# Optimization experiments

Measured on AMD Instinct MI355X. Metric: run time of the kernel, lower is better.

Reference implementation:

```python
import jax, jax.numpy as jnp
import numpy as np

V = 8001
H = 512
B = 64
T = 129  # seq len; model unrolls T-1 steps
EPS = 1e-5
P_DROP = 0.3


def setup_inputs() -> dict:
    key = jax.random.key(0)
    ks = jax.random.split(key, 16)
    s = 1.0 / np.sqrt(H)
    inp = {
        "x": jax.random.randint(ks[0], (B, T), 0, V),
        "emb": jax.random.normal(ks[1], (V, H), jnp.float32) * 0.1,
        "W_ih1": jax.random.normal(ks[2], (4 * H, H), jnp.float32) * s,
        "W_hh1": jax.random.normal(ks[3], (4 * H, H), jnp.float32) * s,
        "b_ih1": jax.random.normal(ks[4], (4 * H,), jnp.float32) * s,
        "b_hh1": jax.random.normal(ks[5], (4 * H,), jnp.float32) * s,
        "gamma1": jnp.ones((H,), jnp.float32),
        "beta1": jnp.zeros((H,), jnp.float32),
        "mask1": (jax.random.bernoulli(ks[6], 1 - P_DROP, (B, H)).astype(jnp.float32) / (1 - P_DROP)),
        "W_ih2": jax.random.normal(ks[7], (4 * H, H), jnp.float32) * s,
        "W_hh2": jax.random.normal(ks[8], (4 * H, H), jnp.float32) * s,
        "b_ih2": jax.random.normal(ks[9], (4 * H,), jnp.float32) * s,
        "b_hh2": jax.random.normal(ks[10], (4 * H,), jnp.float32) * s,
        "gamma2": jnp.ones((H,), jnp.float32),
        "beta2": jnp.zeros((H,), jnp.float32),
        "mask2": (jax.random.bernoulli(ks[11], 1 - P_DROP, (B, H)).astype(jnp.float32) / (1 - P_DROP)),
        "W_dec": jax.random.normal(ks[12], (V, H), jnp.float32) * s,
        "b_dec": jax.random.normal(ks[13], (V,), jnp.float32) * s,
    }
    return inp


def _lstm_cell(xt, h, c, W_ih, W_hh, b_ih, b_hh):
    # PyTorch LSTMCell gate packing: i, f, g, o
    gates = xt @ W_ih.T + b_ih + h @ W_hh.T + b_hh  # [B, 4H]
    i, f, g, o = jnp.split(gates, 4, axis=-1)
    c_new = jax.nn.sigmoid(f) * c + jax.nn.sigmoid(i) * jnp.tanh(g)
    h_new = jax.nn.sigmoid(o) * jnp.tanh(c_new)
    return h_new, c_new


def _batchnorm(h, gamma, beta):
    # training-mode BatchNorm1d: biased batch stats over batch dim
    mu = h.mean(axis=0)
    var = h.var(axis=0)
    return gamma * (h - mu) * jax.lax.rsqrt(var + EPS) + beta


def reference(x, emb, W_ih1, W_hh1, b_ih1, b_hh1, gamma1, beta1, mask1,
              W_ih2, W_hh2, b_ih2, b_hh2, gamma2, beta2, mask2, W_dec, b_dec):
    embed = emb[x]                              # [B, T, H]
    xs = jnp.swapaxes(embed[:, :-1, :], 0, 1)   # [T-1, B, H]

    def step(carry, xt):
        h1, c1, h2, c2 = carry
        h1, c1 = _lstm_cell(xt, h1, c1, W_ih1, W_hh1, b_ih1, b_hh1)
        a = _batchnorm(h1, gamma1, beta1) * mask1
        h2, c2 = _lstm_cell(a, h2, c2, W_ih2, W_hh2, b_ih2, b_hh2)
        b = _batchnorm(h2, gamma2, beta2) * mask2
        out = b @ W_dec.T + b_dec               # [B, V]
        return (h1, c1, h2, c2), out

    z = jnp.zeros((B, H), embed.dtype)
    _, outs = jax.lax.scan(step, (z, z, z, z), xs)  # [T-1, B, V]
    return jnp.transpose(outs, (1, 2, 0))           # [B, V, T-1]
```

## Files before the change

### kernel.cpp

```cpp
#include <hip/hip_runtime.h>

typedef __attribute__((ext_vector_type(8))) short bf16x8;
typedef __attribute__((ext_vector_type(4))) float f32x4;

#define NBATCH 64
#define NH     512
#define NV     8001
#define NVP    8064
#define NSTEP  128
#define NG     2048
#define SLAB   32768

#define OFF_XS    ((size_t)0)
#define SZ_XS     ((size_t)NSTEP*SLAB*2)
#define OFF_WP    (OFF_XS + SZ_XS)
#define SZ_WP     ((size_t)2*2048*1024*2)
#define OFF_WDEC  (OFF_WP + SZ_WP)
#define SZ_WDEC   ((size_t)NVP*NH*2)
#define OFF_BIAS  (OFF_WDEC + SZ_WDEC)
#define SZ_BIAS   ((size_t)2*NG*4)
#define OFF_H1    (OFF_BIAS + SZ_BIAS)
#define SZ_H1     ((size_t)(NSTEP+1)*SLAB*2)
#define OFF_AB    (OFF_H1 + SZ_H1)
#define SZ_AB     ((size_t)NSTEP*SLAB*2)
#define OFF_H2    (OFF_AB + SZ_AB)
#define SZ_H2     ((size_t)(NSTEP+1)*SLAB*2)
#define OFF_BSEQ  (OFF_H2 + SZ_H2)
#define SZ_BSEQ   ((size_t)NSTEP*SLAB*2)
#define OFF_BAR   (OFF_BSEQ + SZ_BSEQ)
#define SZ_BAR    ((size_t)32768)

__device__ __forceinline__ unsigned short f2bf(float x) {
  union { float f; unsigned u; } v; v.f = x;
  unsigned r = v.u + 0x7FFFu + ((v.u >> 16) & 1u);
  return (unsigned short)(r >> 16);
}
__device__ __forceinline__ float sigm(float x) { return 1.f / (1.f + __expf(-x)); }

template <int SLP>
__device__ __forceinline__ void waitflag(unsigned* f) {
  while (__hip_atomic_load(f, __ATOMIC_RELAXED, __HIP_MEMORY_SCOPE_AGENT) < 32u)
    __builtin_amdgcn_s_sleep(SLP);
  asm volatile("" ::: "memory");
}


__global__ void k_xs(const int* __restrict__ x, const float* __restrict__ emb,
                     unsigned short* __restrict__ xs) {
  int idx = blockIdx.x * 256 + threadIdx.x;
  int t = idx >> 12, b = (idx >> 6) & 63, h8 = idx & 63;
  const float* src = emb + (size_t)x[b * 129 + t] * NH + h8 * 8;
  float4 a = *(const float4*)src, c = *(const float4*)(src + 4);
  unsigned short tmp[8] = {f2bf(a.x), f2bf(a.y), f2bf(a.z), f2bf(a.w),
                           f2bf(c.x), f2bf(c.y), f2bf(c.z), f2bf(c.w)};
  *(uint4*)(xs + (size_t)idx * 8) = *(const uint4*)tmp;
}

__global__ void k_wdec(const float* __restrict__ W, unsigned short* __restrict__ wdec) {
  int idx = blockIdx.x * 256 + threadIdx.x;
  int v = idx >> 6, h8 = idx & 63;
  unsigned short tmp[8] = {0, 0, 0, 0, 0, 0, 0, 0};
  if (v < NV) {
    const float* src = W + (size_t)v * NH + h8 * 8;
    float4 a = *(const float4*)src, c = *(const float4*)(src + 4);
    tmp[0] = f2bf(a.x); tmp[1] = f2bf(a.y); tmp[2] = f2bf(a.z); tmp[3] = f2bf(a.w);
    tmp[4] = f2bf(c.x); tmp[5] = f2bf(c.y); tmp[6] = f2bf(c.z); tmp[7] = f2bf(c.w);
  }
  *(uint4*)(wdec + (size_t)idx * 8) = *(const uint4*)tmp;
}

__global__ void k_bias(const float* __restrict__ bi1, const float* __restrict__ bh1,
                       const float* __restrict__ bi2, const float* __restrict__ bh2,
                       float* __restrict__ bias) {
  int i = blockIdx.x * 256 + threadIdx.x;
  bias[i] = (i < NG) ? (bi1[i] + bh1[i]) : (bi2[i - NG] + bh2[i - NG]);
}

__global__ void k_wpack(const float* __restrict__ Wih1, const float* __restrict__ Whh1,
                        const float* __restrict__ Wih2, const float* __restrict__ Whh2,
                        unsigned short* __restrict__ wp) {
  int tid = blockIdx.x * 256 + threadIdx.x;
  int l = tid & 63, g = (tid >> 6) & 3, s = (tid >> 8) & 31, lb = (tid >> 13) & 31, layer = tid >> 18;
  int n = l & 15, q = l >> 4;
  int r = g * NH + lb * 16 + n;
  int k0 = s * 32 + q * 8;
  const float* Wih = layer ? Wih2 : Wih1;
  const float* Whh = layer ? Whh2 : Whh1;
  const float* src = (k0 < NH) ? (Wih + (size_t)r * NH + k0) : (Whh + (size_t)r * NH + (k0 - NH));
  unsigned short tmp[8];
#pragma unroll
  for (int j = 0; j < 8; ++j) tmp[j] = f2bf(src[j]);
  *(uint4*)(wp + (size_t)tid * 8) = *(const uint4*)tmp;
}

__global__ void __launch_bounds__(256, 1)
k_main(const unsigned short* __restrict__ xs, const unsigned short* __restrict__ wpack,
       const float* __restrict__ bias,
       const float* __restrict__ gamma1, const float* __restrict__ beta1, const float* __restrict__ mask1,
       const float* __restrict__ gamma2, const float* __restrict__ beta2, const float* __restrict__ mask2,
       unsigned short* __restrict__ h1q, unsigned short* __restrict__ abq,
       unsigned short* __restrict__ h2q, unsigned short* __restrict__ bseq,
       unsigned* __restrict__ bar,
       const unsigned short* __restrict__ wdec, const float* __restrict__ bdec,
       float* __restrict__ out) {
  __shared__ unsigned short wlds[32 * 4 * 64 * 8];
  __shared__ float red[4][2][16];

  unsigned* done1 = bar;
  unsigned* done2 = bar + 2048;
  unsigned* qcnt  = bar + 4096;

  const int bid = blockIdx.x;
  const int lane = threadIdx.x & 63, w = threadIdx.x >> 6;
  const int q = lane >> 4, n = lane & 15;

  if (bid < 64) {
    const int layer = bid >> 5, lb = bid & 31, f0 = lb * 16;
    const float* gam = layer ? gamma2 : gamma1;
    const float* bet = layer ? beta2 : beta1;
    const float* msk = layer ? mask2 : mask1;
    const float* bias_l = bias + layer * NG;

    {
      const uint4* src = (const uint4*)(wpack + (size_t)bid * (32 * 4 * 64 * 8));
      uint4* dst = (uint4*)wlds;
      for (int i = threadIdx.x; i < 32 * 4 * 64; i += 256) dst[i] = src[i];
    }
    __syncthreads();

    const int m0 = w * 16;
    const float gmv = gam[f0 + n], btv = bet[f0 + n];
    float bias_g[4], mk[4];
#pragma unroll
    for (int g = 0; g < 4; ++g) bias_g[g] = bias_l[g * NH + f0 + n];
#pragma unroll
    for (int r = 0; r < 4; ++r) mk[r] = msk[(m0 + q * 4 + r) * NH + f0 + n];

    float cst[4] = {0.f, 0.f, 0.f, 0.f};

    for (int t = 0; t < NSTEP; ++t) {
      f32x4 acc[4];
#pragma unroll
      for (int g = 0; g < 4; ++g) acc[g] = (f32x4){bias_g[g], bias_g[g], bias_g[g], bias_g[g]};

      if (layer == 0) {
        const unsigned short* rowA0 = xs + (size_t)t * SLAB + (m0 + n) * NH;
#pragma unroll
        for (int s = 0; s < 16; ++s) {
          bf16x8 af = *(const bf16x8*)(rowA0 + s * 32 + q * 8);
#pragma unroll
          for (int g = 0; g < 4; ++g)
            acc[g] = __builtin_amdgcn_mfma_f32_16x16x32_bf16(
                af, *(const bf16x8*)&wlds[((s * 4 + g) * 64 + lane) * 8], acc[g], 0, 0, 0);
        }
        if (t > 0) waitflag<1>(done1 + (t - 1) * 16);
        const unsigned short* rowA1 = h1q + (size_t)t * SLAB + (m0 + n) * NH;
#pragma unroll
        for (int s = 0; s < 16; ++s) {
          bf16x8 af = *(const bf16x8*)(rowA1 + s * 32 + q * 8);
#pragma unroll
          for (int g = 0; g < 4; ++g)
            acc[g] = __builtin_amdgcn_mfma_f32_16x16x32_bf16(
                af, *(const bf16x8*)&wlds[(((s + 16) * 4 + g) * 64 + lane) * 8], acc[g], 0, 0, 0);
        }
      } else {
        if (t > 0) waitflag<1>(done2 + (t - 1) * 16);
        const unsigned short* rowA1 = h2q + (size_t)t * SLAB + (m0 + n) * NH;
#pragma unroll
        for (int s = 0; s < 16; ++s) {
          bf16x8 af = *(const bf16x8*)(rowA1 + s * 32 + q * 8);
#pragma unroll
          for (int g = 0; g < 4; ++g)
            acc[g] = __builtin_amdgcn_mfma_f32_16x16x32_bf16(
                af, *(const bf16x8*)&wlds[(((s + 16) * 4 + g) * 64 + lane) * 8], acc[g], 0, 0, 0);
        }
        waitflag<1>(done1 + t * 16);
        const unsigned short* rowA0 = abq + (size_t)t * SLAB + (m0 + n) * NH;
#pragma unroll
        for (int s = 0; s < 16; ++s) {
          bf16x8 af = *(const bf16x8*)(rowA0 + s * 32 + q * 8);
#pragma unroll
          for (int g = 0; g < 4; ++g)
            acc[g] = __builtin_amdgcn_mfma_f32_16x16x32_bf16(
                af, *(const bf16x8*)&wlds[((s * 4 + g) * 64 + lane) * 8], acc[g], 0, 0, 0);
        }
      }

      float hv[4], sum = 0.f, ssq = 0.f;
#pragma unroll
      for (int r = 0; r < 4; ++r) {
        float ig = sigm(acc[0][r]), fg = sigm(acc[1][r]);
        float gg = tanhf(acc[2][r]), og = sigm(acc[3][r]);
        cst[r] = fg * cst[r] + ig * gg;
        hv[r] = og * tanhf(cst[r]);
        sum += hv[r]; ssq += hv[r] * hv[r];
      }
      sum += __shfl_xor(sum, 16); ssq += __shfl_xor(ssq, 16);
      sum += __shfl_xor(sum, 32); ssq += __shfl_xor(ssq, 32);
      if (q == 0) { red[w][0][n] = sum; red[w][1][n] = ssq; }
      __syncthreads();
      float s1 = red[0][0][n] + red[1][0][n] + red[2][0][n] + red[3][0][n];
      float s2 = red[0][1][n] + red[1][1][n] + red[2][1][n] + red[3][1][n];
      float mu = s1 * (1.f / 64.f);
      float var = s2 * (1.f / 64.f) - mu * mu;
      float rs = rsqrtf(var + 1e-5f);

      unsigned short* hout = ((layer == 0) ? h1q : h2q) + (size_t)(t + 1) * SLAB;
      unsigned short* aout = ((layer == 0) ? abq : bseq) + (size_t)t * SLAB;
#pragma unroll
      for (int r = 0; r < 4; ++r) {
        int row = m0 + q * 4 + r;
        float bn = (hv[r] - mu) * rs * gmv + btv;
        unsigned short hb = f2bf(hv[r]);
        unsigned short av = f2bf(bn * mk[r]);
        __hip_atomic_store(&hout[row * NH + f0 + n], hb, __ATOMIC_RELAXED, __HIP_MEMORY_SCOPE_AGENT);
        __hip_atomic_store(&aout[row * NH + f0 + n], av, __ATOMIC_RELAXED, __HIP_MEMORY_SCOPE_AGENT);
      }

      __syncthreads();
      if (threadIdx.x == 0)
        atomicAdd((layer ? done2 : done1) + t * 16, 1u);
    }
  }

  while (true) {
    unsigned c = 0;
    if (lane == 0) c = atomicAdd(qcnt, 1u);
    c = __shfl(c, 0);
    if (c >= 16384u) break;
    unsigned tc = c >> 12, r = c & 4095u;
    if (r >= 4032u) continue;
    int nb = (int)(r >> 6), b = (int)(r & 63u);
    waitflag<8>(done2 + (tc * 32 + 31) * 16);

    const int n0 = nb * 128;
    f32x4 acc[2][8];
#pragma unroll
    for (int nt = 0; nt < 8; ++nt) {
      int v = n0 + nt * 16 + n;
      float bd = (v < NV) ? bdec[v] : 0.f;
      acc[0][nt] = (f32x4){bd, bd, bd, bd};
      acc[1][nt] = acc[0][nt];
    }
    const unsigned short* arow[2];
#pragma unroll
    for (int mt = 0; mt < 2; ++mt)
      arow[mt] = bseq + ((size_t)(tc * 32 + mt * 16 + n) * NBATCH + b) * NH;
    const unsigned short* brow[8];
#pragma unroll
    for (int nt = 0; nt < 8; ++nt) brow[nt] = wdec + (size_t)(n0 + nt * 16 + n) * NH;

#pragma unroll 4
    for (int s = 0; s < 16; ++s) {
      bf16x8 af[2];
#pragma unroll
      for (int mt = 0; mt < 2; ++mt) af[mt] = *(const bf16x8*)(arow[mt] + s * 32 + q * 8);
#pragma unroll
      for (int nt = 0; nt < 8; ++nt) {
        bf16x8 bf = *(const bf16x8*)(brow[nt] + s * 32 + q * 8);
#pragma unroll
        for (int mt = 0; mt < 2; ++mt)
          acc[mt][nt] = __builtin_amdgcn_mfma_f32_16x16x32_bf16(af[mt], bf, acc[mt][nt], 0, 0, 0);
      }
    }
#pragma unroll
    for (int mt = 0; mt < 2; ++mt)
#pragma unroll
      for (int nt = 0; nt < 8; ++nt) {
        int v = n0 + nt * 16 + n;
        if (v < NV) {
          int t0 = (int)tc * 32 + mt * 16 + q * 4;
          *(f32x4*)(out + ((size_t)b * NV + v) * NSTEP + t0) = acc[mt][nt];
        }
      }
  }
}

extern "C" void kernel_launch(void* const* d_in, const int* in_sizes, int n_in,
                              void* d_out, int out_size, void* d_ws, size_t ws_size,
                              hipStream_t stream) {
  const int*   x     = (const int*)d_in[0];
  const float* emb   = (const float*)d_in[1];
  const float* Wih1  = (const float*)d_in[2];
  const float* Whh1  = (const float*)d_in[3];
  const float* bi1   = (const float*)d_in[4];
  const float* bh1   = (const float*)d_in[5];
  const float* g1    = (const float*)d_in[6];
  const float* be1   = (const float*)d_in[7];
  const float* m1    = (const float*)d_in[8];
  const float* Wih2  = (const float*)d_in[9];
  const float* Whh2  = (const float*)d_in[10];
  const float* bi2   = (const float*)d_in[11];
  const float* bh2   = (const float*)d_in[12];
  const float* g2    = (const float*)d_in[13];
  const float* be2   = (const float*)d_in[14];
  const float* m2    = (const float*)d_in[15];
  const float* Wdec  = (const float*)d_in[16];
  const float* bdec  = (const float*)d_in[17];
  float* out = (float*)d_out;
  char* ws = (char*)d_ws;

  unsigned short* xs    = (unsigned short*)(ws + OFF_XS);
  unsigned short* wp    = (unsigned short*)(ws + OFF_WP);
  unsigned short* wdec  = (unsigned short*)(ws + OFF_WDEC);
  float*          bias  = (float*)(ws + OFF_BIAS);
  unsigned short* h1q   = (unsigned short*)(ws + OFF_H1);
  unsigned short* abq   = (unsigned short*)(ws + OFF_AB);
  unsigned short* h2q   = (unsigned short*)(ws + OFF_H2);
  unsigned short* bseq  = (unsigned short*)(ws + OFF_BSEQ);
  unsigned*       bar   = (unsigned*)(ws + OFF_BAR);

  (void)hipMemsetAsync(h1q, 0, SLAB * 2, stream);
  (void)hipMemsetAsync(h2q, 0, SLAB * 2, stream);
  (void)hipMemsetAsync(bar, 0, SZ_BAR, stream);

  k_xs   <<<dim3(2048), dim3(256), 0, stream>>>(x, emb, xs);
  k_wdec <<<dim3(2016), dim3(256), 0, stream>>>(Wdec, wdec);
  k_bias <<<dim3(16),   dim3(256), 0, stream>>>(bi1, bh1, bi2, bh2, bias);
  k_wpack<<<dim3(2048), dim3(256), 0, stream>>>(Wih1, Whh1, Wih2, Whh2, wp);

  void* kargs[] = {(void*)&xs, (void*)&wp, (void*)&bias,
                   (void*)&g1, (void*)&be1, (void*)&m1,
                   (void*)&g2, (void*)&be2, (void*)&m2,
                   (void*)&h1q, (void*)&abq, (void*)&h2q, (void*)&bseq, (void*)&bar,
                   (void*)&wdec, (void*)&bdec, (void*)&out};
  (void)hipLaunchCooperativeKernel((void*)k_main, dim3(256), dim3(256), kargs, 0, stream);
}
```

Baseline: 1.684 ms.

## Fold prep kernels into cooperative main kernel and refine flag signalling

```diff
diff --git a/kernel.cpp b/kernel.cpp
--- a/kernel.cpp
+++ b/kernel.cpp
@@ -28,7 +28,13 @@
 #define OFF_BSEQ  (OFF_H2 + SZ_H2)
 #define SZ_BSEQ   ((size_t)NSTEP*SLAB*2)
 #define OFF_BAR   (OFF_BSEQ + SZ_BSEQ)
-#define SZ_BAR    ((size_t)32768)
+#define SZ_BAR    ((size_t)65536)
+
+#define F_D1(t)   ((t) * 32)
+#define F_D2(t)   (4096 + (t) * 32)
+#define F_QCNT    8192
+#define F_GBAR    8224
+#define F_DRDY(c) (8320 + (c) * 32)
 
 __device__ __forceinline__ unsigned short f2bf(float x) {
   union { float f; unsigned u; } v; v.f = x;
@@ -44,85 +50,98 @@
   asm volatile("" ::: "memory");
 }
 
-
-__global__ void k_xs(const int* __restrict__ x, const float* __restrict__ emb,
-                     unsigned short* __restrict__ xs) {
-  int idx = blockIdx.x * 256 + threadIdx.x;
-  int t = idx >> 12, b = (idx >> 6) & 63, h8 = idx & 63;
-  const float* src = emb + (size_t)x[b * 129 + t] * NH + h8 * 8;
-  float4 a = *(const float4*)src, c = *(const float4*)(src + 4);
-  unsigned short tmp[8] = {f2bf(a.x), f2bf(a.y), f2bf(a.z), f2bf(a.w),
-                           f2bf(c.x), f2bf(c.y), f2bf(c.z), f2bf(c.w)};
-  *(uint4*)(xs + (size_t)idx * 8) = *(const uint4*)tmp;
-}
-
-__global__ void k_wdec(const float* __restrict__ W, unsigned short* __restrict__ wdec) {
-  int idx = blockIdx.x * 256 + threadIdx.x;
-  int v = idx >> 6, h8 = idx & 63;
-  unsigned short tmp[8] = {0, 0, 0, 0, 0, 0, 0, 0};
-  if (v < NV) {
-    const float* src = W + (size_t)v * NH + h8 * 8;
-    float4 a = *(const float4*)src, c = *(const float4*)(src + 4);
-    tmp[0] = f2bf(a.x); tmp[1] = f2bf(a.y); tmp[2] = f2bf(a.z); tmp[3] = f2bf(a.w);
-    tmp[4] = f2bf(c.x); tmp[5] = f2bf(c.y); tmp[6] = f2bf(c.z); tmp[7] = f2bf(c.w);
-  }
-  *(uint4*)(wdec + (size_t)idx * 8) = *(const uint4*)tmp;
-}
-
-__global__ void k_bias(const float* __restrict__ bi1, const float* __restrict__ bh1,
-                       const float* __restrict__ bi2, const float* __restrict__ bh2,
-                       float* __restrict__ bias) {
-  int i = blockIdx.x * 256 + threadIdx.x;
-  bias[i] = (i < NG) ? (bi1[i] + bh1[i]) : (bi2[i - NG] + bh2[i - NG]);
-}
-
-__global__ void k_wpack(const float* __restrict__ Wih1, const float* __restrict__ Whh1,
-                        const float* __restrict__ Wih2, const float* __restrict__ Whh2,
-                        unsigned short* __restrict__ wp) {
-  int tid = blockIdx.x * 256 + threadIdx.x;
-  int l = tid & 63, g = (tid >> 6) & 3, s = (tid >> 8) & 31, lb = (tid >> 13) & 31, layer = tid >> 18;
-  int n = l & 15, q = l >> 4;
-  int r = g * NH + lb * 16 + n;
-  int k0 = s * 32 + q * 8;
-  const float* Wih = layer ? Wih2 : Wih1;
-  const float* Whh = layer ? Whh2 : Whh1;
-  const float* src = (k0 < NH) ? (Wih + (size_t)r * NH + k0) : (Whh + (size_t)r * NH + (k0 - NH));
-  unsigned short tmp[8];
-#pragma unroll
-  for (int j = 0; j < 8; ++j) tmp[j] = f2bf(src[j]);
-  *(uint4*)(wp + (size_t)tid * 8) = *(const uint4*)tmp;
-}
-
-__global__ void __launch_bounds__(256, 1)
-k_main(const unsigned short* __restrict__ xs, const unsigned short* __restrict__ wpack,
-       const float* __restrict__ bias,
-       const float* __restrict__ gamma1, const float* __restrict__ beta1, const float* __restrict__ mask1,
-       const float* __restrict__ gamma2, const float* __restrict__ beta2, const float* __restrict__ mask2,
-       unsigned short* __restrict__ h1q, unsigned short* __restrict__ abq,
-       unsigned short* __restrict__ h2q, unsigned short* __restrict__ bseq,
-       unsigned* __restrict__ bar,
-       const unsigned short* __restrict__ wdec, const float* __restrict__ bdec,
-       float* __restrict__ out) {
+template <int SLP>
+__device__ __forceinline__ void waitone(unsigned* f) {
+  if (!__hip_atomic_load(f, __ATOMIC_RELAXED, __HIP_MEMORY_SCOPE_AGENT)) {
+    do { __builtin_amdgcn_s_sleep(SLP); }
+    while (!__hip_atomic_load(f, __ATOMIC_RELAXED, __HIP_MEMORY_SCOPE_AGENT));
+  }
+  asm volatile("" ::: "memory");
+}
+
+struct KArgs {
+  const int* x; const float* emb;
+  const float* Wih1; const float* Whh1; const float* bi1; const float* bh1;
+  const float* g1; const float* be1; const float* m1;
+  const float* Wih2; const float* Whh2; const float* bi2; const float* bh2;
+  const float* g2; const float* be2; const float* m2;
+  const float* Wdec; const float* bdec;
+  unsigned short* xs; unsigned short* wp; unsigned short* wdec; float* bias;
+  unsigned short* h1q; unsigned short* abq; unsigned short* h2q; unsigned short* bseq;
+  unsigned* bar; float* out;
+};
+
+__global__ void __launch_bounds__(256, 1) k_main(KArgs a) {
   __shared__ unsigned short wlds[32 * 4 * 64 * 8];
   __shared__ float red[4][2][16];
 
-  unsigned* done1 = bar;
-  unsigned* done2 = bar + 2048;
-  unsigned* qcnt  = bar + 4096;
-
+  unsigned* bar = a.bar;
   const int bid = blockIdx.x;
   const int lane = threadIdx.x & 63, w = threadIdx.x >> 6;
   const int q = lane >> 4, n = lane & 15;
 
+  {
+    const int gtid = bid * 256 + threadIdx.x;
+    if (gtid < 4096)
+      a.bias[gtid] = (gtid < NG) ? (a.bi1[gtid] + a.bh1[gtid])
+                                 : (a.bi2[gtid - NG] + a.bh2[gtid - NG]);
+    if (gtid < 4096) {
+      ((uint4*)a.h1q)[gtid] = (uint4){0, 0, 0, 0};
+      ((uint4*)a.h2q)[gtid] = (uint4){0, 0, 0, 0};
+    }
+    for (int i = gtid; i < 524288; i += 65536) {
+      int t = i >> 12, b = (i >> 6) & 63, h8 = i & 63;
+      const float* src = a.emb + (size_t)a.x[b * 129 + t] * NH + h8 * 8;
+      float4 u = *(const float4*)src, v = *(const float4*)(src + 4);
+      unsigned short tmp[8] = {f2bf(u.x), f2bf(u.y), f2bf(u.z), f2bf(u.w),
+                               f2bf(v.x), f2bf(v.y), f2bf(v.z), f2bf(v.w)};
+      *(uint4*)(a.xs + (size_t)i * 8) = *(const uint4*)tmp;
+    }
+    for (int i = gtid; i < 516096; i += 65536) {
+      int v = i >> 6, h8 = i & 63;
+      unsigned short tmp[8] = {0, 0, 0, 0, 0, 0, 0, 0};
+      if (v < NV) {
+        const float* src = a.Wdec + (size_t)v * NH + h8 * 8;
+        float4 u = *(const float4*)src, vv = *(const float4*)(src + 4);
+        tmp[0] = f2bf(u.x); tmp[1] = f2bf(u.y); tmp[2] = f2bf(u.z); tmp[3] = f2bf(u.w);
+        tmp[4] = f2bf(vv.x); tmp[5] = f2bf(vv.y); tmp[6] = f2bf(vv.z); tmp[7] = f2bf(vv.w);
+      }
+      *(uint4*)(a.wdec + (size_t)i * 8) = *(const uint4*)tmp;
+    }
+    for (int i = gtid; i < 524288; i += 65536) {
+      int l = i & 63, g = (i >> 6) & 3, s = (i >> 8) & 31, lb = (i >> 13) & 31, layer = i >> 18;
+      int nn = l & 15, qq = l >> 4;
+      int r = g * NH + lb * 16 + nn;
+      int k0 = s * 32 + qq * 8;
+      const float* Wih = layer ? a.Wih2 : a.Wih1;
+      const float* Whh = layer ? a.Whh2 : a.Whh1;
+      const float* src = (k0 < NH) ? (Wih + (size_t)r * NH + k0) : (Whh + (size_t)r * NH + (k0 - NH));
+      unsigned short tmp[8];
+#pragma unroll
+      for (int j = 0; j < 8; ++j) tmp[j] = f2bf(src[j]);
+      *(uint4*)(a.wp + (size_t)i * 8) = *(const uint4*)tmp;
+    }
+  }
+  __syncthreads();
+  if (threadIdx.x == 0) {
+    __builtin_amdgcn_fence(__ATOMIC_RELEASE, "agent");
+    __hip_atomic_fetch_add(bar + F_GBAR, 1u, __ATOMIC_RELAXED, __HIP_MEMORY_SCOPE_AGENT);
+    while (__hip_atomic_load(bar + F_GBAR, __ATOMIC_RELAXED, __HIP_MEMORY_SCOPE_AGENT) < 256u)
+      __builtin_amdgcn_s_sleep(8);
+  }
+  __syncthreads();
+  asm volatile("" ::: "memory");
+
   if (bid < 64) {
     const int layer = bid >> 5, lb = bid & 31, f0 = lb * 16;
-    const float* gam = layer ? gamma2 : gamma1;
-    const float* bet = layer ? beta2 : beta1;
-    const float* msk = layer ? mask2 : mask1;
-    const float* bias_l = bias + layer * NG;
+    const float* gam = layer ? a.g2 : a.g1;
+    const float* bet = layer ? a.be2 : a.be1;
+    const float* msk = layer ? a.m2 : a.m1;
+    const float* bias_l = a.bias + layer * NG;
+    unsigned* myflag = bar + (layer ? F_D2(0) : F_D1(0));
 
     {
-      const uint4* src = (const uint4*)(wpack + (size_t)bid * (32 * 4 * 64 * 8));
+      const uint4* src = (const uint4*)(a.wp + (size_t)bid * (32 * 4 * 64 * 8));
       uint4* dst = (uint4*)wlds;
       for (int i = threadIdx.x; i < 32 * 4 * 64; i += 256) dst[i] = src[i];
     }
@@ -144,7 +163,7 @@
       for (int g = 0; g < 4; ++g) acc[g] = (f32x4){bias_g[g], bias_g[g], bias_g[g], bias_g[g]};
 
       if (layer == 0) {
-        const unsigned short* rowA0 = xs + (size_t)t * SLAB + (m0 + n) * NH;
+        const unsigned short* rowA0 = a.xs + (size_t)t * SLAB + (m0 + n) * NH;
 #pragma unroll
         for (int s = 0; s < 16; ++s) {
           bf16x8 af = *(const bf16x8*)(rowA0 + s * 32 + q * 8);
@@ -153,8 +172,8 @@
             acc[g] = __builtin_amdgcn_mfma_f32_16x16x32_bf16(
                 af, *(const bf16x8*)&wlds[((s * 4 + g) * 64 + lane) * 8], acc[g], 0, 0, 0);
         }
-        if (t > 0) waitflag<1>(done1 + (t - 1) * 16);
-        const unsigned short* rowA1 = h1q + (size_t)t * SLAB + (m0 + n) * NH;
+        if (t > 0) waitflag<1>(bar + F_D1(t - 1));
+        const unsigned short* rowA1 = a.h1q + (size_t)t * SLAB + (m0 + n) * NH;
 #pragma unroll
         for (int s = 0; s < 16; ++s) {
           bf16x8 af = *(const bf16x8*)(rowA1 + s * 32 + q * 8);
@@ -164,8 +183,8 @@
                 af, *(const bf16x8*)&wlds[(((s + 16) * 4 + g) * 64 + lane) * 8], acc[g], 0, 0, 0);
         }
       } else {
-        if (t > 0) waitflag<1>(done2 + (t - 1) * 16);
-        const unsigned short* rowA1 = h2q + (size_t)t * SLAB + (m0 + n) * NH;
+        if (t > 0) waitflag<1>(bar + F_D2(t - 1));
+        const unsigned short* rowA1 = a.h2q + (size_t)t * SLAB + (m0 + n) * NH;
 #pragma unroll
         for (int s = 0; s < 16; ++s) {
           bf16x8 af = *(const bf16x8*)(rowA1 + s * 32 + q * 8);
@@ -174,8 +193,8 @@
             acc[g] = __builtin_amdgcn_mfma_f32_16x16x32_bf16(
                 af, *(const bf16x8*)&wlds[(((s + 16) * 4 + g) * 64 + lane) * 8], acc[g], 0, 0, 0);
         }
-        waitflag<1>(done1 + t * 16);
-        const unsigned short* rowA0 = abq + (size_t)t * SLAB + (m0 + n) * NH;
+        waitflag<1>(bar + F_D1(t));
+        const unsigned short* rowA0 = a.abq + (size_t)t * SLAB + (m0 + n) * NH;
 #pragma unroll
         for (int s = 0; s < 16; ++s) {
           bf16x8 af = *(const bf16x8*)(rowA0 + s * 32 + q * 8);
@@ -205,8 +224,8 @@
       float var = s2 * (1.f / 64.f) - mu * mu;
       float rs = rsqrtf(var + 1e-5f);
 
-      unsigned short* hout = ((layer == 0) ? h1q : h2q) + (size_t)(t + 1) * SLAB;
-      unsigned short* aout = ((layer == 0) ? abq : bseq) + (size_t)t * SLAB;
+      unsigned short* hout = ((layer == 0) ? a.h1q : a.h2q) + (size_t)(t + 1) * SLAB;
+      unsigned short* aout = ((layer == 0) ? a.abq : a.bseq) + (size_t)t * SLAB;
 #pragma unroll
       for (int r = 0; r < 4; ++r) {
         int row = m0 + q * 4 + r;
@@ -218,37 +237,42 @@
       }
 
       __syncthreads();
-      if (threadIdx.x == 0)
-        atomicAdd((layer ? done2 : done1) + t * 16, 1u);
+      if (threadIdx.x == 0) {
+        unsigned old = __hip_atomic_fetch_add(myflag + t * 32, 1u,
+                                              __ATOMIC_RELAXED, __HIP_MEMORY_SCOPE_AGENT);
+        if (layer == 1 && old == 31u && (t & 31) == 31)
+          __hip_atomic_store(bar + F_DRDY(t >> 5), 1u,
+                             __ATOMIC_RELAXED, __HIP_MEMORY_SCOPE_AGENT);
+      }
     }
   }
 
   while (true) {
     unsigned c = 0;
-    if (lane == 0) c = atomicAdd(qcnt, 1u);
+    if (lane == 0) c = atomicAdd(bar + F_QCNT, 1u);
     c = __shfl(c, 0);
     if (c >= 16384u) break;
     unsigned tc = c >> 12, r = c & 4095u;
     if (r >= 4032u) continue;
     int nb = (int)(r >> 6), b = (int)(r & 63u);
-    waitflag<8>(done2 + (tc * 32 + 31) * 16);
+    waitone<127>(bar + F_DRDY(tc));
 
     const int n0 = nb * 128;
     f32x4 acc[2][8];
 #pragma unroll
     for (int nt = 0; nt < 8; ++nt) {
       int v = n0 + nt * 16 + n;
-      float bd = (v < NV) ? bdec[v] : 0.f;
+      float bd = (v < NV) ? a.bdec[v] : 0.f;
       acc[0][nt] = (f32x4){bd, bd, bd, bd};
       acc[1][nt] = acc[0][nt];
     }
     const unsigned short* arow[2];
 #pragma unroll
     for (int mt = 0; mt < 2; ++mt)
-      arow[mt] = bseq + ((size_t)(tc * 32 + mt * 16 + n) * NBATCH + b) * NH;
+      arow[mt] = a.bseq + ((size_t)(tc * 32 + mt * 16 + n) * NBATCH + b) * NH;
     const unsigned short* brow[8];
 #pragma unroll
-    for (int nt = 0; nt < 8; ++nt) brow[nt] = wdec + (size_t)(n0 + nt * 16 + n) * NH;
+    for (int nt = 0; nt < 8; ++nt) brow[nt] = a.wdec + (size_t)(n0 + nt * 16 + n) * NH;
 
 #pragma unroll 4
     for (int s = 0; s < 16; ++s) {
@@ -270,7 +294,7 @@
         int v = n0 + nt * 16 + n;
         if (v < NV) {
           int t0 = (int)tc * 32 + mt * 16 + q * 4;
-          *(f32x4*)(out + ((size_t)b * NV + v) * NSTEP + t0) = acc[mt][nt];
+          *(f32x4*)(a.out + ((size_t)b * NV + v) * NSTEP + t0) = acc[mt][nt];
         }
       }
   }
@@ -279,50 +303,40 @@
 extern "C" void kernel_launch(void* const* d_in, const int* in_sizes, int n_in,
                               void* d_out, int out_size, void* d_ws, size_t ws_size,
                               hipStream_t stream) {
-  const int*   x     = (const int*)d_in[0];
-  const float* emb   = (const float*)d_in[1];
-  const float* Wih1  = (const float*)d_in[2];
-  const float* Whh1  = (const float*)d_in[3];
-  const float* bi1   = (const float*)d_in[4];
-  const float* bh1   = (const float*)d_in[5];
-  const float* g1    = (const float*)d_in[6];
-  const float* be1   = (const float*)d_in[7];
-  const float* m1    = (const float*)d_in[8];
-  const float* Wih2  = (const float*)d_in[9];
-  const float* Whh2  = (const float*)d_in[10];
-  const float* bi2   = (const float*)d_in[11];
-  const float* bh2   = (const float*)d_in[12];
-  const float* g2    = (const float*)d_in[13];
-  const float* be2   = (const float*)d_in[14];
-  const float* m2    = (const float*)d_in[15];
-  const float* Wdec  = (const float*)d_in[16];
-  const float* bdec  = (const float*)d_in[17];
-  float* out = (float*)d_out;
   char* ws = (char*)d_ws;
 
-  unsigned short* xs    = (unsigned short*)(ws + OFF_XS);
-  unsigned short* wp    = (unsigned short*)(ws + OFF_WP);
-  unsigned short* wdec  = (unsigned short*)(ws + OFF_WDEC);
-  float*          bias  = (float*)(ws + OFF_BIAS);
-  unsigned short* h1q   = (unsigned short*)(ws + OFF_H1);
-  unsigned short* abq   = (unsigned short*)(ws + OFF_AB);
-  unsigned short* h2q   = (unsigned short*)(ws + OFF_H2);
-  unsigned short* bseq  = (unsigned short*)(ws + OFF_BSEQ);
-  unsigned*       bar   = (unsigned*)(ws + OFF_BAR);
-
-  (void)hipMemsetAsync(h1q, 0, SLAB * 2, stream);
-  (void)hipMemsetAsync(h2q, 0, SLAB * 2, stream);
-  (void)hipMemsetAsync(bar, 0, SZ_BAR, stream);
-
-  k_xs   <<<dim3(2048), dim3(256), 0, stream>>>(x, emb, xs);
-  k_wdec <<<dim3(2016), dim3(256), 0, stream>>>(Wdec, wdec);
-  k_bias <<<dim3(16),   dim3(256), 0, stream>>>(bi1, bh1, bi2, bh2, bias);
-  k_wpack<<<dim3(2048), dim3(256), 0, stream>>>(Wih1, Whh1, Wih2, Whh2, wp);
-
-  void* kargs[] = {(void*)&xs, (void*)&wp, (void*)&bias,
-                   (void*)&g1, (void*)&be1, (void*)&m1,
-                   (void*)&g2, (void*)&be2, (void*)&m2,
-                   (void*)&h1q, (void*)&abq, (void*)&h2q, (void*)&bseq, (void*)&bar,
-                   (void*)&wdec, (void*)&bdec, (void*)&out};
+  KArgs a;
+  a.x    = (const int*)d_in[0];
+  a.emb  = (const float*)d_in[1];
+  a.Wih1 = (const float*)d_in[2];
+  a.Whh1 = (const float*)d_in[3];
+  a.bi1  = (const float*)d_in[4];
+  a.bh1  = (const float*)d_in[5];
+  a.g1   = (const float*)d_in[6];
+  a.be1  = (const float*)d_in[7];
+  a.m1   = (const float*)d_in[8];
+  a.Wih2 = (const float*)d_in[9];
+  a.Whh2 = (const float*)d_in[10];
+  a.bi2  = (const float*)d_in[11];
+  a.bh2  = (const float*)d_in[12];
+  a.g2   = (const float*)d_in[13];
+  a.be2  = (const float*)d_in[14];
+  a.m2   = (const float*)d_in[15];
+  a.Wdec = (const float*)d_in[16];
+  a.bdec = (const float*)d_in[17];
+  a.xs   = (unsigned short*)(ws + OFF_XS);
+  a.wp   = (unsigned short*)(ws + OFF_WP);
+  a.wdec = (unsigned short*)(ws + OFF_WDEC);
+  a.bias = (float*)(ws + OFF_BIAS);
+  a.h1q  = (unsigned short*)(ws + OFF_H1);
+  a.abq  = (unsigned short*)(ws + OFF_AB);
+  a.h2q  = (unsigned short*)(ws + OFF_H2);
+  a.bseq = (unsigned short*)(ws + OFF_BSEQ);
+  a.bar  = (unsigned*)(ws + OFF_BAR);
+  a.out  = (float*)d_out;
+
+  (void)hipMemsetAsync(a.bar, 0, SZ_BAR, stream);
+
+  void* kargs[] = {(void*)&a};
   (void)hipLaunchCooperativeKernel((void*)k_main, dim3(256), dim3(256), kargs, 0, stream);
 }
```

Result: faster. 1.641 ms (-2.6%).
